# Kernel tuning notes

Hardware: AMD Instinct MI355X
Metric: run time of the kernel (lower is better)

The kernel has to match this reference:

```python
import jax, jax.numpy as jnp
import numpy as np
import math

HIDDEN = 256
HEADS = 8
HEAD_DIM = HIDDEN // HEADS
SCALE = math.sqrt(HEAD_DIM)


def setup_inputs() -> dict:
    key = jax.random.key(0)
    ks = jax.random.split(key, 10)
    B, N = 2, 4096
    x = jax.random.normal(ks[0], (B, N, HIDDEN), dtype=jnp.float32)
    pos = jax.random.normal(ks[1], (B, N, 3), dtype=jnp.float32)
    s = 1.0 / math.sqrt(HIDDEN)
    Wq = jax.random.normal(ks[2], (HIDDEN, HIDDEN), dtype=jnp.float32) * s
    bq = jnp.zeros((HIDDEN,), dtype=jnp.float32)
    Wk = jax.random.normal(ks[3], (HIDDEN, HIDDEN), dtype=jnp.float32) * s
    bk = jnp.zeros((HIDDEN,), dtype=jnp.float32)
    Wv = jax.random.normal(ks[4], (HIDDEN, HIDDEN), dtype=jnp.float32) * s
    bv = jnp.zeros((HIDDEN,), dtype=jnp.float32)
    Wo = jax.random.normal(ks[5], (HIDDEN, HIDDEN), dtype=jnp.float32) * s
    bo = jnp.zeros((HIDDEN,), dtype=jnp.float32)
    return {"x": x, "pos": pos, "Wq": Wq, "bq": bq, "Wk": Wk, "bk": bk,
            "Wv": Wv, "bv": bv, "Wo": Wo, "bo": bo}


def _pairwise_dist(pos):
    # Euclidean cdist via the norm trick; clip for numerical safety.
    sq = jnp.sum(pos * pos, axis=-1)  # [B, N]
    d2 = sq[:, :, None] + sq[:, None, :] - 2.0 * jnp.einsum('bic,bjc->bij', pos, pos)
    return jnp.sqrt(jnp.maximum(d2, 0.0))  # [B, N, N]


def reference(x, pos, Wq, bq, Wk, bk, Wv, bv, Wo, bo):
    B, N, _ = x.shape
    # projections -> [B, H, N, Dh]
    def split_heads(t):
        return t.reshape(B, N, HEADS, HEAD_DIM).transpose(0, 2, 1, 3)
    q = split_heads(x @ Wq.T + bq)
    k = split_heads(x @ Wk.T + bk)
    v = split_heads(x @ Wv.T + bv)
    scores = jnp.einsum('bhid,bhjd->bhij', q, k) / SCALE
    dist_bias = -_pairwise_dist(pos) / 10.0  # [B, N, N]
    scores = scores + dist_bias[:, None, :, :]
    attn = jax.nn.softmax(scores, axis=-1)
    out = jnp.einsum('bhij,bhjd->bhid', attn, v)
    out = out.transpose(0, 2, 1, 3).reshape(B, N, HIDDEN)
    return out @ Wo.T + bo
```

## Files before the change

kernel.cpp:

```cpp
#include <hip/hip_runtime.h>

#define BATCH 2
#define SEQ   4096
#define HID   256
#define NHEAD 8
#define DH    32
#define THR_L2 11.5f
#define QSCALE 0.25501639769925074f
#define BIASC (-0.14426950408889634f)

typedef __attribute__((ext_vector_type(8))) _Float16 half8;
typedef __attribute__((ext_vector_type(4))) _Float16 half4;
typedef __attribute__((ext_vector_type(2))) __fp16   fp16x2;
typedef __attribute__((ext_vector_type(4))) float    f32x4;

__device__ __forceinline__ float fast_exp2(float x) {
    return __builtin_amdgcn_exp2f(x);
}

__global__ void cvt_f32_f16(const float* __restrict__ src,
                            _Float16* __restrict__ dst, int n) {
    int i = (blockIdx.x * blockDim.x + threadIdx.x) * 4;
    if (i >= n) return;
    f32x4 v = *reinterpret_cast<const f32x4*>(src + i);
    half4 h;
#pragma unroll
    for (int c = 0; c < 4; ++c) h[c] = (_Float16)v[c];
    *reinterpret_cast<half4*>(dst + i) = h;
}

__global__ void cvt_w4(const float* __restrict__ a, const float* __restrict__ b,
                       const float* __restrict__ c, const float* __restrict__ d,
                       _Float16* __restrict__ dst) {
    const float* srcs[4] = {a, b, c, d};
    const float* s = srcs[blockIdx.y];
    const int i = (blockIdx.x * blockDim.x + threadIdx.x) * 4;
    f32x4 v = *reinterpret_cast<const f32x4*>(s + i);
    half4 h;
#pragma unroll
    for (int k = 0; k < 4; ++k) h[k] = (_Float16)v[k];
    *reinterpret_cast<half4*>(dst + (size_t)blockIdx.y * HID * HID + i) = h;
}

__global__ __launch_bounds__(256) void qkv_proj(
    const _Float16* __restrict__ xh, const _Float16* __restrict__ Wh,
    const float* __restrict__ bq, const float* __restrict__ bk,
    const float* __restrict__ bv,
    _Float16* __restrict__ Qh, _Float16* __restrict__ Kh,
    _Float16* __restrict__ Vt)
{
    const int z   = blockIdx.z;
    const int m0  = blockIdx.x * 64;
    const int n0  = blockIdx.y * 64;
    const int tid = threadIdx.x;
    const int w   = tid >> 6, lane = tid & 63;
    const int lr  = lane & 15, lg = lane >> 4;
    const int wr  = (w >> 1) * 32, wc = (w & 1) * 32;

    const _Float16* Wp = Wh + (size_t)z * HID * HID;
    const float* bias = (z == 0) ? bq : (z == 1) ? bk : bv;

    f32x4 acc[2][2] = {};
    const int ar = m0 + wr + lr;
    const int br = n0 + wc + lr;
#pragma unroll
    for (int ks = 0; ks < 8; ++ks) {
        const int ko = ks * 32 + lg * 8;
        half8 a0 = *reinterpret_cast<const half8*>(xh + (size_t)ar * HID + ko);
        half8 a1 = *reinterpret_cast<const half8*>(xh + (size_t)(ar + 16) * HID + ko);
        half8 b0 = *reinterpret_cast<const half8*>(Wp + (size_t)br * HID + ko);
        half8 b1 = *reinterpret_cast<const half8*>(Wp + (size_t)(br + 16) * HID + ko);
        acc[0][0] = __builtin_amdgcn_mfma_f32_16x16x32_f16(a0, b0, acc[0][0], 0, 0, 0);
        acc[0][1] = __builtin_amdgcn_mfma_f32_16x16x32_f16(a0, b1, acc[0][1], 0, 0, 0);
        acc[1][0] = __builtin_amdgcn_mfma_f32_16x16x32_f16(a1, b0, acc[1][0], 0, 0, 0);
        acc[1][1] = __builtin_amdgcn_mfma_f32_16x16x32_f16(a1, b1, acc[1][1], 0, 0, 0);
    }
#pragma unroll
    for (int mf = 0; mf < 2; ++mf)
#pragma unroll
    for (int nf = 0; nf < 2; ++nf)
#pragma unroll
    for (int r = 0; r < 4; ++r) {
        const int m  = m0 + wr + mf * 16 + lg * 4 + r;
        const int o  = n0 + wc + nf * 16 + lr;
        const int bb = m >> 12, nn = m & (SEQ - 1);
        const int hh = o >> 5,  dd = o & (DH - 1);
        float v = acc[mf][nf][r] + bias[o];
        if (z == 0) {
            Qh[(((size_t)(bb * NHEAD + hh) * SEQ) + nn) * DH + dd] =
                (_Float16)(v * QSCALE);
        } else if (z == 1) {
            Kh[(((size_t)(bb * NHEAD + hh) * SEQ) + nn) * DH + dd] = (_Float16)v;
        } else {
            Vt[(((size_t)(bb * NHEAD + hh) * DH) + dd) * SEQ + nn] = (_Float16)v;
        }
    }
}

__global__ __launch_bounds__(512, 4) void attn_kernel(
    const _Float16* __restrict__ Qh, const _Float16* __restrict__ Kh,
    const _Float16* __restrict__ Vt, const float* __restrict__ pos,
    _Float16* __restrict__ AO)
{
    __shared__ __align__(16) float pi4[16][4];
    __shared__ __align__(16) float pj4[512][4];
    __shared__ __align__(16) float biasL[16][516];
    __shared__ __align__(16) _Float16 Pl[NHEAD][16 * 72];
    __shared__ __align__(16) float xposeL[NHEAD][16];

    const int b    = blockIdx.y;
    const int i0   = blockIdx.x * 16;
    const int tid  = threadIdx.x;
    const int w    = tid >> 6;
    const int lane = tid & 63;
    const int lr   = lane & 15, lg = lane >> 4;

    if (tid < 16) {
        const float* p = pos + (size_t)(b * SEQ + i0 + tid) * 3;
        float x = p[0], y = p[1], z = p[2];
        pi4[tid][0] = x; pi4[tid][1] = y; pi4[tid][2] = z;
        pi4[tid][3] = x * x + y * y + z * z;
    }

    const size_t bhh = (size_t)(b * NHEAD + w);
    const _Float16* Qbase = Qh + (bhh * SEQ + i0) * DH;
    const _Float16* Kl  = Kh + bhh * SEQ * DH + (size_t)lr * DH + lg * 8;
    const _Float16* Vl0 = Vt + bhh * DH * SEQ + (size_t)lr * SEQ + lg * 8;
    const _Float16* Vl1 = Vt + bhh * DH * SEQ + (size_t)(16 + lr) * SEQ + lg * 8;

    const half8 aq = *reinterpret_cast<const half8*>(Qbase + (size_t)lr * DH + lg * 8);

    f32x4 acc0 = {}, acc1 = {};
    float mrun = -1e30f, lsum = 0.f;

    char* PlW = (char*)&Pl[w][0];

    for (int ch = 0; ch < SEQ / 512; ++ch) {
        __syncthreads();
        {
            const float* p = pos + (size_t)(b * SEQ + ch * 512 + tid) * 3;
            float x = p[0], y = p[1], z = p[2];
            pj4[tid][0] = x; pj4[tid][1] = y; pj4[tid][2] = z;
            pj4[tid][3] = x * x + y * y + z * z;
        }
        __syncthreads();
        {
            const int br  = tid & 15;
            const int c0  = (tid >> 4) * 16;
            const float xi = pi4[br][0], yi = pi4[br][1], zi = pi4[br][2], si = pi4[br][3];
#pragma unroll
            for (int k4 = 0; k4 < 4; ++k4) {
                f32x4 o;
#pragma unroll
                for (int k = 0; k < 4; ++k) {
                    const float* pj = &pj4[c0 + k4 * 4 + k][0];
                    float dot = xi * pj[0] + yi * pj[1] + zi * pj[2];
                    float d2  = si + pj[3] - 2.f * dot;
                    o[k] = BIASC * sqrtf(fmaxf(d2, 0.f));
                }
                *reinterpret_cast<f32x4*>(&biasL[br][c0 + k4 * 4]) = o;
            }
        }
        __syncthreads();

        half8 k8[4];
#pragma unroll
        for (int cf = 0; cf < 4; ++cf)
            k8[cf] = *reinterpret_cast<const half8*>(
                Kl + (size_t)(ch * 512 + cf * 16) * DH);

#pragma unroll 2
        for (int s = 0; s < 8; ++s) {
            const int j0 = ch * 512 + s * 64;

            half8 bva = *reinterpret_cast<const half8*>(Vl0 + j0);
            half8 bvb = *reinterpret_cast<const half8*>(Vl1 + j0);
            half8 bvc = *reinterpret_cast<const half8*>(Vl0 + j0 + 32);
            half8 bvd = *reinterpret_cast<const half8*>(Vl1 + j0 + 32);

            f32x4 vv[4];
#pragma unroll
            for (int cf = 0; cf < 4; ++cf) {
                f32x4 cb = *reinterpret_cast<const f32x4*>(
                    &biasL[lr][s * 64 + cf * 16 + lg * 4]);
                vv[cf] = __builtin_amdgcn_mfma_f32_16x16x32_f16(k8[cf], aq, cb, 0, 0, 0);
            }

            half8 kn[4];
            if (s < 7) {
#pragma unroll
                for (int cf = 0; cf < 4; ++cf)
                    kn[cf] = *reinterpret_cast<const half8*>(
                        Kl + (size_t)(j0 + 64 + cf * 16) * DH);
            }

            float tmax = fmaxf(fmaxf(vv[0][0], vv[0][1]), vv[0][2]);
            tmax = fmaxf(fmaxf(tmax, vv[0][3]), vv[1][0]);
            tmax = fmaxf(fmaxf(tmax, vv[1][1]), vv[1][2]);
            tmax = fmaxf(fmaxf(tmax, vv[1][3]), vv[2][0]);
            tmax = fmaxf(fmaxf(tmax, vv[2][1]), vv[2][2]);
            tmax = fmaxf(fmaxf(tmax, vv[2][3]), vv[3][0]);
            tmax = fmaxf(fmaxf(tmax, vv[3][1]), vv[3][2]);
            tmax = fmaxf(tmax, vv[3][3]);

            if (!__all(tmax <= mrun + THR_L2)) {
                float tm = tmax;
                tm = fmaxf(tm, __shfl_xor(tm, 16, 64));
                tm = fmaxf(tm, __shfl_xor(tm, 32, 64));
                const float mnew  = fmaxf(mrun, tm);
                const float alpha = fast_exp2(mrun - mnew);
                if (lane < 16) xposeL[w][lane] = alpha;
                f32x4 a4 = *reinterpret_cast<const f32x4*>(&xposeL[w][lg * 4]);
                lsum *= alpha;
                mrun = mnew;
                acc0 *= a4;
                acc1 *= a4;
            }

#pragma unroll
            for (int cf = 0; cf < 4; ++cf) {
                float p0 = fast_exp2(vv[cf][0] - mrun);
                float p1 = fast_exp2(vv[cf][1] - mrun);
                float p2 = fast_exp2(vv[cf][2] - mrun);
                float p3 = fast_exp2(vv[cf][3] - mrun);
                lsum += (p0 + p1) + (p2 + p3);
                fp16x2 ha = __builtin_amdgcn_cvt_pkrtz(p0, p1);
                fp16x2 hb = __builtin_amdgcn_cvt_pkrtz(p2, p3);
                unsigned int wlo = __builtin_bit_cast(unsigned int, ha);
                unsigned int whi = __builtin_bit_cast(unsigned int, hb);
                unsigned long long wq =
                    (unsigned long long)wlo | ((unsigned long long)whi << 32);
                *reinterpret_cast<unsigned long long*>(
                    PlW + lr * 144 + (cf * 16 + lg * 4) * 2) = wq;
            }

            half8 pa0 = *reinterpret_cast<const half8*>(PlW + lr * 144 + (lg * 8) * 2);
            half8 pa1 = *reinterpret_cast<const half8*>(PlW + lr * 144 + (32 + lg * 8) * 2);
            acc0 = __builtin_amdgcn_mfma_f32_16x16x32_f16(pa0, bva, acc0, 0, 0, 0);
            acc1 = __builtin_amdgcn_mfma_f32_16x16x32_f16(pa0, bvb, acc1, 0, 0, 0);
            acc0 = __builtin_amdgcn_mfma_f32_16x16x32_f16(pa1, bvc, acc0, 0, 0, 0);
            acc1 = __builtin_amdgcn_mfma_f32_16x16x32_f16(pa1, bvd, acc1, 0, 0, 0);

            if (s < 7) {
#pragma unroll
                for (int cf = 0; cf < 4; ++cf) k8[cf] = kn[cf];
            }
        }
    }

    lsum += __shfl_xor(lsum, 16, 64);
    lsum += __shfl_xor(lsum, 32, 64);
    const float inv = 1.f / lsum;
    if (lane < 16) xposeL[w][lane] = inv;
    f32x4 i4 = *reinterpret_cast<const f32x4*>(&xposeL[w][lg * 4]);
#pragma unroll
    for (int t = 0; t < 4; ++t) {
        const size_t row = (size_t)(b * SEQ + i0 + lg * 4 + t) * HID + w * DH;
        AO[row + lr]      = (_Float16)(acc0[t] * i4[t]);
        AO[row + 16 + lr] = (_Float16)(acc1[t] * i4[t]);
    }
}

__global__ __launch_bounds__(256) void out_proj(
    const _Float16* __restrict__ AO, const _Float16* __restrict__ Woh,
    const float* __restrict__ bo, float* __restrict__ out)
{
    const int m0  = blockIdx.x * 64;
    const int n0  = blockIdx.y * 64;
    const int tid = threadIdx.x;
    const int w   = tid >> 6, lane = tid & 63;
    const int lr  = lane & 15, lg = lane >> 4;
    const int wr  = (w >> 1) * 32, wc = (w & 1) * 32;

    f32x4 acc[2][2] = {};
    const int ar = m0 + wr + lr;
    const int br = n0 + wc + lr;
#pragma unroll
    for (int ks = 0; ks < 8; ++ks) {
        const int ko = ks * 32 + lg * 8;
        half8 a0 = *reinterpret_cast<const half8*>(AO + (size_t)ar * HID + ko);
        half8 a1 = *reinterpret_cast<const half8*>(AO + (size_t)(ar + 16) * HID + ko);
        half8 b0 = *reinterpret_cast<const half8*>(Woh + (size_t)br * HID + ko);
        half8 b1 = *reinterpret_cast<const half8*>(Woh + (size_t)(br + 16) * HID + ko);
        acc[0][0] = __builtin_amdgcn_mfma_f32_16x16x32_f16(a0, b0, acc[0][0], 0, 0, 0);
        acc[0][1] = __builtin_amdgcn_mfma_f32_16x16x32_f16(a0, b1, acc[0][1], 0, 0, 0);
        acc[1][0] = __builtin_amdgcn_mfma_f32_16x16x32_f16(a1, b0, acc[1][0], 0, 0, 0);
        acc[1][1] = __builtin_amdgcn_mfma_f32_16x16x32_f16(a1, b1, acc[1][1], 0, 0, 0);
    }
#pragma unroll
    for (int mf = 0; mf < 2; ++mf)
#pragma unroll
    for (int nf = 0; nf < 2; ++nf)
#pragma unroll
    for (int r = 0; r < 4; ++r) {
        const int m = m0 + wr + mf * 16 + lg * 4 + r;
        const int o = n0 + wc + nf * 16 + lr;
        out[(size_t)m * HID + o] = acc[mf][nf][r] + bo[o];
    }
}

extern "C" void kernel_launch(void* const* d_in, const int* in_sizes, int n_in,
                              void* d_out, int out_size, void* d_ws, size_t ws_size,
                              hipStream_t stream)
{
    const float* x   = (const float*)d_in[0];
    const float* pos = (const float*)d_in[1];
    const float* Wq  = (const float*)d_in[2];
    const float* bq  = (const float*)d_in[3];
    const float* Wk  = (const float*)d_in[4];
    const float* bk  = (const float*)d_in[5];
    const float* Wv  = (const float*)d_in[6];
    const float* bv  = (const float*)d_in[7];
    const float* Wo  = (const float*)d_in[8];
    const float* bo  = (const float*)d_in[9];
    float* out = (float*)d_out;

    char* ws = (char*)d_ws;
    _Float16* Qh = (_Float16*)(ws);
    _Float16* Kh = (_Float16*)(ws + (4  << 20));
    _Float16* Vt = (_Float16*)(ws + (8  << 20));
    _Float16* xh = (_Float16*)(ws + (12 << 20));
    _Float16* AO = xh;
    _Float16* Wh = (_Float16*)(ws + (16 << 20));

    const int NX = BATCH * SEQ * HID;
    const int NW = HID * HID;
    cvt_f32_f16<<<NX / 1024, 256, 0, stream>>>(x, xh, NX);
    cvt_w4<<<dim3(NW / 1024, 4), 256, 0, stream>>>(Wq, Wk, Wv, Wo, Wh);

    qkv_proj<<<dim3(BATCH * SEQ / 64, HID / 64, 3), 256, 0, stream>>>(
        xh, Wh, bq, bk, bv, Qh, Kh, Vt);

    attn_kernel<<<dim3(SEQ / 16, BATCH), 512, 0, stream>>>(Qh, Kh, Vt, pos, AO);

    out_proj<<<dim3(BATCH * SEQ / 64, HID / 64), 256, 0, stream>>>(
        AO, Wh + 3 * NW, bo, out);
}
```

Baseline: 235.7 us.

## Double-buffer K/V register tiles across chunks and raise MFMA wave priority

Restructures the attention inner loop into a helper that prefetches the next tile's K and V fragments into ping-pong register buffers, with prefetch running across chunk boundaries. Before, V was loaded in the same step it was consumed and K prefetch stopped at each chunk end. The MFMA sections are wrapped in s_setprio to favour matrix issue, and the max reduction is rebalanced into a shallower tree. The extra live registers (two K and two V buffer sets) may pressure occupancy under launch_bounds(512,4). The last tile also wraps around and issues a redundant load.

```diff
diff --git a/kernel.cpp b/kernel.cpp
--- a/kernel.cpp
+++ b/kernel.cpp
@@ -97,6 +97,85 @@
     }
 }
 
+__device__ __forceinline__ void attn_tile(
+    int t,
+    const _Float16* __restrict__ Kl, const _Float16* __restrict__ Vl0,
+    const _Float16* __restrict__ Vl1,
+    half8 aq, half8 (&kc)[4], half8 (&kn)[4], half8 (&vc)[4], half8 (&vn)[4],
+    const float* __restrict__ biasRow, char* PlW, float* xw,
+    float& mrun, float& lsum, f32x4& acc0, f32x4& acc1, int lane, int lg)
+{
+    const int tn = (t + 1) & (SEQ / 64 - 1);
+
+#pragma unroll
+    for (int cf = 0; cf < 4; ++cf)
+        kn[cf] = *reinterpret_cast<const half8*>(
+            Kl + (size_t)(tn * 64 + cf * 16) * DH);
+    vn[0] = *reinterpret_cast<const half8*>(Vl0 + tn * 64);
+    vn[1] = *reinterpret_cast<const half8*>(Vl1 + tn * 64);
+    vn[2] = *reinterpret_cast<const half8*>(Vl0 + tn * 64 + 32);
+    vn[3] = *reinterpret_cast<const half8*>(Vl1 + tn * 64 + 32);
+
+    const int sb = (t & 7) * 64;
+    f32x4 vv[4];
+    __builtin_amdgcn_s_setprio(1);
+#pragma unroll
+    for (int cf = 0; cf < 4; ++cf) {
+        f32x4 cb = *reinterpret_cast<const f32x4*>(biasRow + sb + cf * 16 + lg * 4);
+        vv[cf] = __builtin_amdgcn_mfma_f32_16x16x32_f16(kc[cf], aq, cb, 0, 0, 0);
+    }
+    __builtin_amdgcn_s_setprio(0);
+
+    float m0 = fmaxf(fmaxf(vv[0][0], vv[0][1]), vv[0][2]);
+    float m1 = fmaxf(fmaxf(vv[0][3], vv[1][0]), vv[1][1]);
+    float m2 = fmaxf(fmaxf(vv[1][2], vv[1][3]), vv[2][0]);
+    float m3 = fmaxf(fmaxf(vv[2][1], vv[2][2]), vv[2][3]);
+    float m4 = fmaxf(fmaxf(vv[3][0], vv[3][1]), vv[3][2]);
+    float tmax = fmaxf(fmaxf(fmaxf(m0, m1), fmaxf(m2, m3)),
+                       fmaxf(m4, vv[3][3]));
+
+    if (!__all(tmax <= mrun + THR_L2)) {
+        float tm = tmax;
+        tm = fmaxf(tm, __shfl_xor(tm, 16, 64));
+        tm = fmaxf(tm, __shfl_xor(tm, 32, 64));
+        const float mnew  = fmaxf(mrun, tm);
+        const float alpha = fast_exp2(mrun - mnew);
+        if (lane < 16) xw[lane] = alpha;
+        f32x4 a4 = *reinterpret_cast<const f32x4*>(&xw[lg * 4]);
+        lsum *= alpha;
+        mrun = mnew;
+        acc0 *= a4;
+        acc1 *= a4;
+    }
+
+    const int lr = lane & 15;
+#pragma unroll
+    for (int cf = 0; cf < 4; ++cf) {
+        float p0 = fast_exp2(vv[cf][0] - mrun);
+        float p1 = fast_exp2(vv[cf][1] - mrun);
+        float p2 = fast_exp2(vv[cf][2] - mrun);
+        float p3 = fast_exp2(vv[cf][3] - mrun);
+        lsum += (p0 + p1) + (p2 + p3);
+        fp16x2 ha = __builtin_amdgcn_cvt_pkrtz(p0, p1);
+        fp16x2 hb = __builtin_amdgcn_cvt_pkrtz(p2, p3);
+        unsigned int wlo = __builtin_bit_cast(unsigned int, ha);
+        unsigned int whi = __builtin_bit_cast(unsigned int, hb);
+        unsigned long long wq =
+            (unsigned long long)wlo | ((unsigned long long)whi << 32);
+        *reinterpret_cast<unsigned long long*>(
+            PlW + lr * 144 + (cf * 16 + lg * 4) * 2) = wq;
+    }
+
+    half8 pa0 = *reinterpret_cast<const half8*>(PlW + lr * 144 + (lg * 8) * 2);
+    half8 pa1 = *reinterpret_cast<const half8*>(PlW + lr * 144 + (32 + lg * 8) * 2);
+    __builtin_amdgcn_s_setprio(1);
+    acc0 = __builtin_amdgcn_mfma_f32_16x16x32_f16(pa0, vc[0], acc0, 0, 0, 0);
+    acc1 = __builtin_amdgcn_mfma_f32_16x16x32_f16(pa0, vc[1], acc1, 0, 0, 0);
+    acc0 = __builtin_amdgcn_mfma_f32_16x16x32_f16(pa1, vc[2], acc0, 0, 0, 0);
+    acc1 = __builtin_amdgcn_mfma_f32_16x16x32_f16(pa1, vc[3], acc1, 0, 0, 0);
+    __builtin_amdgcn_s_setprio(0);
+}
+
 __global__ __launch_bounds__(512, 4) void attn_kernel(
     const _Float16* __restrict__ Qh, const _Float16* __restrict__ Kh,
     const _Float16* __restrict__ Vt, const float* __restrict__ pos,
@@ -134,6 +213,17 @@
     float mrun = -1e30f, lsum = 0.f;
 
     char* PlW = (char*)&Pl[w][0];
+    float* xw = &xposeL[w][0];
+    const float* biasRow = &biasL[lr][0];
+
+    half8 kA[4], kB[4], vA[4], vB[4];
+#pragma unroll
+    for (int cf = 0; cf < 4; ++cf)
+        kA[cf] = *reinterpret_cast<const half8*>(Kl + (size_t)(cf * 16) * DH);
+    vA[0] = *reinterpret_cast<const half8*>(Vl0);
+    vA[1] = *reinterpret_cast<const half8*>(Vl1);
+    vA[2] = *reinterpret_cast<const half8*>(Vl0 + 32);
+    vA[3] = *reinterpret_cast<const half8*>(Vl1 + 32);
 
     for (int ch = 0; ch < SEQ / 512; ++ch) {
         __syncthreads();
@@ -163,96 +253,20 @@
         }
         __syncthreads();
 
-        half8 k8[4];
-#pragma unroll
-        for (int cf = 0; cf < 4; ++cf)
-            k8[cf] = *reinterpret_cast<const half8*>(
-                Kl + (size_t)(ch * 512 + cf * 16) * DH);
-
-#pragma unroll 2
-        for (int s = 0; s < 8; ++s) {
-            const int j0 = ch * 512 + s * 64;
-
-            half8 bva = *reinterpret_cast<const half8*>(Vl0 + j0);
-            half8 bvb = *reinterpret_cast<const half8*>(Vl1 + j0);
-            half8 bvc = *reinterpret_cast<const half8*>(Vl0 + j0 + 32);
-            half8 bvd = *reinterpret_cast<const half8*>(Vl1 + j0 + 32);
-
-            f32x4 vv[4];
-#pragma unroll
-            for (int cf = 0; cf < 4; ++cf) {
-                f32x4 cb = *reinterpret_cast<const f32x4*>(
-                    &biasL[lr][s * 64 + cf * 16 + lg * 4]);
-                vv[cf] = __builtin_amdgcn_mfma_f32_16x16x32_f16(k8[cf], aq, cb, 0, 0, 0);
-            }
-
-            half8 kn[4];
-            if (s < 7) {
-#pragma unroll
-                for (int cf = 0; cf < 4; ++cf)
-                    kn[cf] = *reinterpret_cast<const half8*>(
-                        Kl + (size_t)(j0 + 64 + cf * 16) * DH);
-            }
-
-            float tmax = fmaxf(fmaxf(vv[0][0], vv[0][1]), vv[0][2]);
-            tmax = fmaxf(fmaxf(tmax, vv[0][3]), vv[1][0]);
-            tmax = fmaxf(fmaxf(tmax, vv[1][1]), vv[1][2]);
-            tmax = fmaxf(fmaxf(tmax, vv[1][3]), vv[2][0]);
-            tmax = fmaxf(fmaxf(tmax, vv[2][1]), vv[2][2]);
-            tmax = fmaxf(fmaxf(tmax, vv[2][3]), vv[3][0]);
-            tmax = fmaxf(fmaxf(tmax, vv[3][1]), vv[3][2]);
-            tmax = fmaxf(tmax, vv[3][3]);
-
-            if (!__all(tmax <= mrun + THR_L2)) {
-                float tm = tmax;
-                tm = fmaxf(tm, __shfl_xor(tm, 16, 64));
-                tm = fmaxf(tm, __shfl_xor(tm, 32, 64));
-                const float mnew  = fmaxf(mrun, tm);
-                const float alpha = fast_exp2(mrun - mnew);
-                if (lane < 16) xposeL[w][lane] = alpha;
-                f32x4 a4 = *reinterpret_cast<const f32x4*>(&xposeL[w][lg * 4]);
-                lsum *= alpha;
-                mrun = mnew;
-                acc0 *= a4;
-                acc1 *= a4;
-            }
-
-#pragma unroll
-            for (int cf = 0; cf < 4; ++cf) {
-                float p0 = fast_exp2(vv[cf][0] - mrun);
-                float p1 = fast_exp2(vv[cf][1] - mrun);
-                float p2 = fast_exp2(vv[cf][2] - mrun);
-                float p3 = fast_exp2(vv[cf][3] - mrun);
-                lsum += (p0 + p1) + (p2 + p3);
-                fp16x2 ha = __builtin_amdgcn_cvt_pkrtz(p0, p1);
-                fp16x2 hb = __builtin_amdgcn_cvt_pkrtz(p2, p3);
-                unsigned int wlo = __builtin_bit_cast(unsigned int, ha);
-                unsigned int whi = __builtin_bit_cast(unsigned int, hb);
-                unsigned long long wq =
-                    (unsigned long long)wlo | ((unsigned long long)whi << 32);
-                *reinterpret_cast<unsigned long long*>(
-                    PlW + lr * 144 + (cf * 16 + lg * 4) * 2) = wq;
-            }
-
-            half8 pa0 = *reinterpret_cast<const half8*>(PlW + lr * 144 + (lg * 8) * 2);
-            half8 pa1 = *reinterpret_cast<const half8*>(PlW + lr * 144 + (32 + lg * 8) * 2);
-            acc0 = __builtin_amdgcn_mfma_f32_16x16x32_f16(pa0, bva, acc0, 0, 0, 0);
-            acc1 = __builtin_amdgcn_mfma_f32_16x16x32_f16(pa0, bvb, acc1, 0, 0, 0);
-            acc0 = __builtin_amdgcn_mfma_f32_16x16x32_f16(pa1, bvc, acc0, 0, 0, 0);
-            acc1 = __builtin_amdgcn_mfma_f32_16x16x32_f16(pa1, bvd, acc1, 0, 0, 0);
-
-            if (s < 7) {
-#pragma unroll
-                for (int cf = 0; cf < 4; ++cf) k8[cf] = kn[cf];
-            }
+        for (int s = 0; s < 4; ++s) {
+            const int t = ch * 8 + s * 2;
+            attn_tile(t,     Kl, Vl0, Vl1, aq, kA, kB, vA, vB,
+                      biasRow, PlW, xw, mrun, lsum, acc0, acc1, lane, lg);
+            attn_tile(t + 1, Kl, Vl0, Vl1, aq, kB, kA, vB, vA,
+                      biasRow, PlW, xw, mrun, lsum, acc0, acc1, lane, lg);
         }
     }
 
     lsum += __shfl_xor(lsum, 16, 64);
     lsum += __shfl_xor(lsum, 32, 64);
     const float inv = 1.f / lsum;
-    if (lane < 16) xposeL[w][lane] = inv;
-    f32x4 i4 = *reinterpret_cast<const f32x4*>(&xposeL[w][lg * 4]);
+    if (lane < 16) xw[lane] = inv;
+    f32x4 i4 = *reinterpret_cast<const f32x4*>(&xw[lg * 4]);
 #pragma unroll
     for (int t = 0; t < 4; ++t) {
         const size_t row = (size_t)(b * SEQ + i0 + lg * 4 + t) * HID + w * DH;
```

Measured after the change: 236.7 us. About the same (+0.4%).
